# Kernel optimization log

Measured on AMD Instinct MI355X. Metric: run time of the kernel, lower is better.

The kernel has to match this reference:

```python
import jax, jax.numpy as jnp
import numpy as np

BINS = 10
LOSS_WEIGHT = 1.0
N, C = 524288, 80


def setup_inputs() -> dict:
    key = jax.random.key(0)
    k1, k2 = jax.random.split(key)
    pred = jax.random.normal(k1, (N, C), dtype=jnp.float32)
    target = jax.random.randint(k2, (N, C), 0, 2).astype(jnp.float32)
    label_weight = jnp.ones((N, C), dtype=jnp.float32)
    return {"pred": pred, "target": target, "label_weight": label_weight}


def reference(pred, target, label_weight):
    # gradient magnitude g = |sigmoid(pred).detach() - target|, in [0, 1)
    g = jnp.abs(jax.nn.sigmoid(jax.lax.stop_gradient(pred)) - target)
    valid = (label_weight > 0)
    validf = valid.astype(pred.dtype)
    tot = jnp.maximum(jnp.sum(validf), 1.0)

    # edges[i] = i/BINS (last edge nudged by 1e-6) -> bin index = floor(g*BINS), clipped
    idx = jnp.clip(jnp.floor(g * BINS).astype(jnp.int32), 0, BINS - 1)
    counts = jnp.zeros((BINS,), dtype=pred.dtype).at[idx.ravel()].add(validf.ravel())
    nonempty = counts > 0
    n = jnp.sum(nonempty.astype(pred.dtype))

    w_per_bin = jnp.where(nonempty, tot / jnp.maximum(counts, 1.0), 0.0)
    weights = w_per_bin[idx] * validf
    weights = weights / jnp.maximum(n, 1.0)
    weights = jax.lax.stop_gradient(weights)  # weights carry no grad in the original

    # binary_cross_entropy_with_logits, elementwise, stable form
    bce = jnp.maximum(pred, 0.0) - pred * target + jnp.log1p(jnp.exp(-jnp.abs(pred)))
    loss = jnp.sum(weights * bce) / tot
    return loss * LOSS_WEIGHT
```

## Files before the change

kernel.cpp:

```cpp
#include <hip/hip_runtime.h>
#include <math.h>

#define BINS 10
#define NBLOCKS 2048
#define THREADS 256

struct Partial {
    float        sum[BINS];
    unsigned int cnt[BINS];
};

__device__ __forceinline__ void accum_one(float x, float t, float w,
                                          float (&s)[BINS], unsigned int (&c)[BINS]) {
    const bool valid = (w > 0.0f);
    float ax  = fabsf(x);
    float e   = __expf(-ax);
    float inv = __builtin_amdgcn_rcpf(1.0f + e);
    float sig = (x >= 0.0f) ? inv : (1.0f - inv);
    float g   = fabsf(sig - t);
    int idx   = (int)(g * 10.0f);
    idx = idx > (BINS - 1) ? (BINS - 1) : idx;
    float bce = fmaxf(x, 0.0f) - x * t + __logf(1.0f + e);
    bce = valid ? bce : 0.0f;
    const unsigned int one = valid ? 1u : 0u;
#pragma unroll
    for (int b = 0; b < BINS; ++b) {
        const bool m = (idx == b);
        s[b] += m ? bce : 0.0f;
        c[b] += m ? one : 0u;
    }
}

__global__ __launch_bounds__(THREADS) void ghmc_main(const float* __restrict__ pred,
                                                     const float* __restrict__ target,
                                                     const float* __restrict__ lw,
                                                     Partial* __restrict__ part,
                                                     long long total) {
    float        s[BINS];
    unsigned int c[BINS];
#pragma unroll
    for (int b = 0; b < BINS; ++b) { s[b] = 0.0f; c[b] = 0u; }

    const int tid = threadIdx.x;
    const long long nvec   = total >> 2;
    const long long stride = (long long)gridDim.x * THREADS;

    for (long long i = (long long)blockIdx.x * THREADS + tid; i < nvec; i += stride) {
        float4 p = reinterpret_cast<const float4*>(pred)[i];
        float4 t = reinterpret_cast<const float4*>(target)[i];
        float4 w = reinterpret_cast<const float4*>(lw)[i];
        accum_one(p.x, t.x, w.x, s, c);
        accum_one(p.y, t.y, w.y, s, c);
        accum_one(p.z, t.z, w.z, s, c);
        accum_one(p.w, t.w, w.w, s, c);
    }

    const long long base = nvec << 2;
    const int rem = (int)(total - base);
    if (blockIdx.x == 0 && tid < rem)
        accum_one(pred[base + tid], target[base + tid], lw[base + tid], s, c);

#pragma unroll
    for (int b = 0; b < BINS; ++b) {
#pragma unroll
        for (int off = 32; off; off >>= 1) {
            s[b] += __shfl_xor(s[b], off, 64);
            c[b] += __shfl_xor(c[b], off, 64);
        }
    }

    __shared__ float        ls[THREADS / 64][BINS];
    __shared__ unsigned int lc[THREADS / 64][BINS];
    const int wid  = tid >> 6;
    const int lane = tid & 63;
    if (lane == 0) {
#pragma unroll
        for (int b = 0; b < BINS; ++b) { ls[wid][b] = s[b]; lc[wid][b] = c[b]; }
    }
    __syncthreads();

    if (tid < BINS) {
        float sb = 0.0f; unsigned int cb = 0u;
#pragma unroll
        for (int w2 = 0; w2 < THREADS / 64; ++w2) { sb += ls[w2][tid]; cb += lc[w2][tid]; }
        part[blockIdx.x].sum[tid] = sb;
        part[blockIdx.x].cnt[tid] = cb;
    }
}

__global__ __launch_bounds__(THREADS) void ghmc_finalize(const Partial* __restrict__ part,
                                                         float* __restrict__ out,
                                                         int nblocks) {
    double             acc[BINS];
    unsigned long long cn[BINS];
#pragma unroll
    for (int b = 0; b < BINS; ++b) { acc[b] = 0.0; cn[b] = 0ull; }

    const int tid = threadIdx.x;
    for (int i = tid; i < nblocks; i += THREADS) {
#pragma unroll
        for (int b = 0; b < BINS; ++b) {
            acc[b] += (double)part[i].sum[b];
            cn[b]  += (unsigned long long)part[i].cnt[b];
        }
    }

#pragma unroll
    for (int b = 0; b < BINS; ++b) {
#pragma unroll
        for (int off = 32; off; off >>= 1) {
            acc[b] += __shfl_xor(acc[b], off, 64);
            cn[b]  += __shfl_xor(cn[b], off, 64);
        }
    }

    __shared__ double             lds_s[THREADS / 64][BINS];
    __shared__ unsigned long long lds_c[THREADS / 64][BINS];
    const int wid  = tid >> 6;
    const int lane = tid & 63;
    if (lane == 0) {
#pragma unroll
        for (int b = 0; b < BINS; ++b) { lds_s[wid][b] = acc[b]; lds_c[wid][b] = cn[b]; }
    }
    __syncthreads();

    if (tid == 0) {
        double loss = 0.0;
        int n = 0;
        for (int b = 0; b < BINS; ++b) {
            double sb = 0.0; unsigned long long cb = 0ull;
            for (int w2 = 0; w2 < THREADS / 64; ++w2) { sb += lds_s[w2][b]; cb += lds_c[w2][b]; }
            if (cb) { loss += sb / (double)cb; ++n; }
        }
        double denom = (n > 0) ? (double)n : 1.0;
        out[0] = (float)(loss / denom);
    }
}

extern "C" void kernel_launch(void* const* d_in, const int* in_sizes, int n_in,
                              void* d_out, int out_size, void* d_ws, size_t ws_size,
                              hipStream_t stream) {
    const float* pred   = (const float*)d_in[0];
    const float* target = (const float*)d_in[1];
    const float* lw     = (const float*)d_in[2];
    float* out = (float*)d_out;
    Partial* part = (Partial*)d_ws;
    const long long total = (long long)in_sizes[0];

    ghmc_main<<<NBLOCKS, THREADS, 0, stream>>>(pred, target, lw, part, total);
    ghmc_finalize<<<1, THREADS, 0, stream>>>(part, out, NBLOCKS);
}
```

Measured before the change: 458.3 us.

## Bin by logit thresholds with cumulative counts via ballot and prefetch loads

Replaces the sigmoid-based bin index with comparisons of the signed logit (x*(1-2t)) against precomputed logit thresholds. It accumulates cumulative (suffix) sums and counts per threshold and recovers per-bin values by differencing in the finalize kernel. Counts are taken wave-wide with ballot/popcount, so the per-lane count shuffle reduction is dropped. The main loop also software-pipelines the next float4 loads ahead of the compute. This removes the reciprocal and the sigmoid work, at the risk of threshold-boundary mismatches and float cancellation in the differenced sums.

```diff
diff --git a/kernel.cpp b/kernel.cpp
--- a/kernel.cpp
+++ b/kernel.cpp
@@ -10,25 +10,38 @@
     unsigned int cnt[BINS];
 };
 
+__device__ __constant__ const float TH[9] = {
+    -2.1972245773f, -1.3862943611f, -0.8472978604f, -0.4054651081f, 0.0f,
+     0.4054651081f,  0.8472978604f,  1.3862943611f,  2.1972245773f
+};
+
 __device__ __forceinline__ void accum_one(float x, float t, float w,
-                                          float (&s)[BINS], unsigned int (&c)[BINS]) {
-    const bool valid = (w > 0.0f);
-    float ax  = fabsf(x);
+                                          float (&A)[BINS], unsigned int (&C)[BINS]) {
+    float m2t = -2.0f * t;
+    float s   = __builtin_fmaf(m2t, x, x);
+    float ax  = __builtin_fabsf(x);
     float e   = __expf(-ax);
-    float inv = __builtin_amdgcn_rcpf(1.0f + e);
-    float sig = (x >= 0.0f) ? inv : (1.0f - inv);
-    float g   = fabsf(sig - t);
-    int idx   = (int)(g * 10.0f);
-    idx = idx > (BINS - 1) ? (BINS - 1) : idx;
-    float bce = fmaxf(x, 0.0f) - x * t + __logf(1.0f + e);
+    float lg  = __logf(1.0f + e);
+    float bce = fmaxf(s, 0.0f) + lg;
+    bool valid = (w > 0.0f);
     bce = valid ? bce : 0.0f;
-    const unsigned int one = valid ? 1u : 0u;
+    float sv = valid ? s : -1e30f;
+    A[0] += bce;
+    C[0] += (unsigned int)__popcll(__ballot(valid));
 #pragma unroll
-    for (int b = 0; b < BINS; ++b) {
-        const bool m = (idx == b);
-        s[b] += m ? bce : 0.0f;
-        c[b] += m ? one : 0u;
+    for (int k = 1; k < BINS; ++k) {
+        bool m = (sv >= TH[k - 1]);
+        A[k] += m ? bce : 0.0f;
+        C[k] += (unsigned int)__popcll(__ballot(m));
     }
+}
+
+__device__ __forceinline__ void accum4(const float4& p, const float4& t, const float4& w,
+                                       float (&A)[BINS], unsigned int (&C)[BINS]) {
+    accum_one(p.x, t.x, w.x, A, C);
+    accum_one(p.y, t.y, w.y, A, C);
+    accum_one(p.z, t.z, w.z, A, C);
+    accum_one(p.w, t.w, w.w, A, C);
 }
 
 __global__ __launch_bounds__(THREADS) void ghmc_main(const float* __restrict__ pred,
@@ -36,37 +49,39 @@
                                                      const float* __restrict__ lw,
                                                      Partial* __restrict__ part,
                                                      long long total) {
-    float        s[BINS];
-    unsigned int c[BINS];
+    float        A[BINS];
+    unsigned int C[BINS];
 #pragma unroll
-    for (int b = 0; b < BINS; ++b) { s[b] = 0.0f; c[b] = 0u; }
+    for (int b = 0; b < BINS; ++b) { A[b] = 0.0f; C[b] = 0u; }
 
     const int tid = threadIdx.x;
     const long long nvec   = total >> 2;
     const long long stride = (long long)gridDim.x * THREADS;
+    const float4* __restrict__ P = reinterpret_cast<const float4*>(pred);
+    const float4* __restrict__ T = reinterpret_cast<const float4*>(target);
+    const float4* __restrict__ W = reinterpret_cast<const float4*>(lw);
 
-    for (long long i = (long long)blockIdx.x * THREADS + tid; i < nvec; i += stride) {
-        float4 p = reinterpret_cast<const float4*>(pred)[i];
-        float4 t = reinterpret_cast<const float4*>(target)[i];
-        float4 w = reinterpret_cast<const float4*>(lw)[i];
-        accum_one(p.x, t.x, w.x, s, c);
-        accum_one(p.y, t.y, w.y, s, c);
-        accum_one(p.z, t.z, w.z, s, c);
-        accum_one(p.w, t.w, w.w, s, c);
+    long long i = (long long)blockIdx.x * THREADS + tid;
+    const bool have = (i < nvec);
+    float4 pa, ta, wa;
+    if (have) { pa = P[i]; ta = T[i]; wa = W[i]; }
+    for (long long j = i + stride; j < nvec; j += stride) {
+        float4 pb = P[j], tb = T[j], wb = W[j];
+        accum4(pa, ta, wa, A, C);
+        pa = pb; ta = tb; wa = wb;
     }
+    if (have) accum4(pa, ta, wa, A, C);
 
     const long long base = nvec << 2;
     const int rem = (int)(total - base);
     if (blockIdx.x == 0 && tid < rem)
-        accum_one(pred[base + tid], target[base + tid], lw[base + tid], s, c);
+        accum_one(pred[base + tid], target[base + tid], lw[base + tid], A, C);
 
 #pragma unroll
     for (int b = 0; b < BINS; ++b) {
 #pragma unroll
-        for (int off = 32; off; off >>= 1) {
-            s[b] += __shfl_xor(s[b], off, 64);
-            c[b] += __shfl_xor(c[b], off, 64);
-        }
+        for (int off = 32; off; off >>= 1)
+            A[b] += __shfl_xor(A[b], off, 64);
     }
 
     __shared__ float        ls[THREADS / 64][BINS];
@@ -75,7 +90,7 @@
     const int lane = tid & 63;
     if (lane == 0) {
 #pragma unroll
-        for (int b = 0; b < BINS; ++b) { ls[wid][b] = s[b]; lc[wid][b] = c[b]; }
+        for (int b = 0; b < BINS; ++b) { ls[wid][b] = A[b]; lc[wid][b] = C[b]; }
     }
     __syncthreads();
 
@@ -104,7 +119,6 @@
             cn[b]  += (unsigned long long)part[i].cnt[b];
         }
     }
-
 #pragma unroll
     for (int b = 0; b < BINS; ++b) {
 #pragma unroll
@@ -125,12 +139,20 @@
     __syncthreads();
 
     if (tid == 0) {
+        double pS[BINS + 1];
+        double pC[BINS + 1];
+        for (int b = 0; b < BINS; ++b) {
+            double sb = 0.0; unsigned long long cb = 0ull;
+            for (int w2 = 0; w2 < THREADS / 64; ++w2) { sb += lds_s[w2][b]; cb += lds_c[w2][b]; }
+            pS[b] = sb; pC[b] = (double)cb;
+        }
+        pS[BINS] = 0.0; pC[BINS] = 0.0;
         double loss = 0.0;
         int n = 0;
         for (int b = 0; b < BINS; ++b) {
-            double sb = 0.0; unsigned long long cb = 0ull;
-            for (int w2 = 0; w2 < THREADS / 64; ++w2) { sb += lds_s[w2][b]; cb += lds_c[w2][b]; }
-            if (cb) { loss += sb / (double)cb; ++n; }
+            double cb = pC[b] - pC[b + 1];
+            double sb = pS[b] - pS[b + 1];
+            if (cb > 0.0) { loss += sb / cb; ++n; }
         }
         double denom = (n > 0) ? (double)n : 1.0;
         out[0] = (float)(loss / denom);
```

Result: faster. 437.0 us (-4.7%).
